# Kernel optimization log

Hardware: AMD Instinct MI355X
Metric: run time of the kernel (lower is better)

The kernel has to match this reference:

```python
import jax, jax.numpy as jnp
import numpy as np
import math

N_HEAD = 16
EPS = 1e-5
GELU_C = math.sqrt(2.0 / math.pi)

def _layernorm(v, w):
    # LN with weight only (bias=None), matching the module's quirky constructor
    mu = jnp.mean(v, axis=-1, keepdims=True)
    var = jnp.mean(jnp.square(v - mu), axis=-1, keepdims=True)
    return (v - mu) * jax.lax.rsqrt(var + EPS) * w

def _new_gelu(x):
    return 0.5 * x * (1.0 + jnp.tanh(GELU_C * (x + 0.044715 * x ** 3)))

def setup_inputs() -> dict:
    key = jax.random.key(0)
    k1, k2, k3, k4 = jax.random.split(key, 4)
    B, T, C = 2, 2048, 2048
    x = jax.random.normal(k1, (B, T, C), dtype=jnp.float32)
    w_qkv = jax.random.normal(k2, (C, 3 * C), dtype=jnp.float32) * 0.02
    w1 = jax.random.normal(k3, (C, 4 * C), dtype=jnp.float32) * 0.02
    w2 = jax.random.normal(k4, (4 * C, C), dtype=jnp.float32) * 0.02
    ln_w = jnp.ones((C,), dtype=jnp.float32)
    return {"x": x, "w_qkv": w_qkv, "w1": w1, "w2": w2, "ln_w": ln_w}

def reference(x, w_qkv, w1, w2, ln_w):
    B, T, C = x.shape
    H = N_HEAD
    D = C // H
    # --- attention branch (pre-LN, shared ln weight) ---
    h = _layernorm(x, ln_w)
    qkv = h @ w_qkv  # [B,T,3C]
    q, k, v = jnp.split(qkv, 3, axis=-1)
    q = q.reshape(B, T, H, D)
    k = k.reshape(B, T, H, D)
    v = v.reshape(B, T, H, D)
    scale = 1.0 / math.sqrt(D)
    att = jnp.einsum('bthd,bshd->bhts', q, k) * scale  # [B,H,T,T]
    causal = jnp.tril(jnp.ones((T, T), dtype=bool))
    att = jnp.where(causal, att, -jnp.inf)
    att = jax.nn.softmax(att, axis=-1)
    attn_out = jnp.einsum('bhts,bshd->bthd', att, v).reshape(B, T, C)
    x = x + attn_out  # note: no output projection in this module
    # --- MLP branch (same ln weight reused) ---
    h2 = _layernorm(x, ln_w)
    mlp = _new_gelu(h2 @ w1) @ w2
    return x + mlp
```

## Files before the change

kernel.cpp:

```cpp
#include <hip/hip_runtime.h>
#include <hip/hip_bf16.h>
#include <math.h>

typedef __bf16 BF16;
typedef __attribute__((ext_vector_type(8))) __bf16 bf16x8;
typedef __attribute__((ext_vector_type(4))) float f32x4;

__device__ __forceinline__ void gld_lds16(const void* g, void* l) {
    __builtin_amdgcn_global_load_lds(
        (__attribute__((address_space(1))) void*)(const void*)g,
        (__attribute__((address_space(3))) void*)l, 16, 0, 0);
}

template <int N> __device__ __forceinline__ void vmwait() {
    asm volatile("s_waitcnt vmcnt(%0)" :: "i"(N));
}

__global__ __launch_bounds__(256) void lnorm(const float* __restrict__ x,
                                             const float* __restrict__ w,
                                             BF16* __restrict__ out) {
    const int row = blockIdx.x, tid = threadIdx.x;
    const float* xr = x + (size_t)row * 2048;
    float4 a = *(const float4*)(xr + tid * 8);
    float4 b = *(const float4*)(xr + tid * 8 + 4);
    float s1 = a.x + a.y + a.z + a.w + b.x + b.y + b.z + b.w;
    float s2 = a.x*a.x + a.y*a.y + a.z*a.z + a.w*a.w +
               b.x*b.x + b.y*b.y + b.z*b.z + b.w*b.w;
    #pragma unroll
    for (int off = 32; off; off >>= 1) {
        s1 += __shfl_xor(s1, off);
        s2 += __shfl_xor(s2, off);
    }
    __shared__ float red[8];
    const int l = tid & 63, wv = tid >> 6;
    if (l == 0) { red[wv] = s1; red[4 + wv] = s2; }
    __syncthreads();
    s1 = red[0] + red[1] + red[2] + red[3];
    s2 = red[4] + red[5] + red[6] + red[7];
    const float mean = s1 * (1.0f / 2048.0f);
    const float var  = s2 * (1.0f / 2048.0f) - mean * mean;
    const float rstd = rsqrtf(var + 1e-5f);
    float4 wa = *(const float4*)(w + tid * 8);
    float4 wb = *(const float4*)(w + tid * 8 + 4);
    bf16x8 o;
    o[0] = (BF16)((a.x - mean) * rstd * wa.x);
    o[1] = (BF16)((a.y - mean) * rstd * wa.y);
    o[2] = (BF16)((a.z - mean) * rstd * wa.z);
    o[3] = (BF16)((a.w - mean) * rstd * wa.w);
    o[4] = (BF16)((b.x - mean) * rstd * wb.x);
    o[5] = (BF16)((b.y - mean) * rstd * wb.y);
    o[6] = (BF16)((b.z - mean) * rstd * wb.z);
    o[7] = (BF16)((b.w - mean) * rstd * wb.w);
    *(bf16x8*)(out + (size_t)row * 2048 + tid * 8) = o;
}

__global__ __launch_bounds__(256) void wtrans(const float* __restrict__ W,
                                              BF16* __restrict__ Wt,
                                              int K, int N) {
    __shared__ BF16 tile[32][33];
    const int n0 = blockIdx.x * 32, k0 = blockIdx.y * 32;
    const int tx = threadIdx.x, ty = threadIdx.y;
    #pragma unroll
    for (int i = 0; i < 4; i++)
        tile[ty + 8 * i][tx] = (BF16)W[(size_t)(k0 + ty + 8 * i) * N + n0 + tx];
    __syncthreads();
    #pragma unroll
    for (int i = 0; i < 4; i++)
        Wt[(size_t)(n0 + ty + 8 * i) * K + k0 + tx] = tile[tx][ty + 8 * i];
}

__global__ __launch_bounds__(256) void vtrans(const BF16* __restrict__ qkv,
                                              BF16* __restrict__ vT) {
    __shared__ BF16 tile[32][33];
    const int t0 = blockIdx.x * 32, d0 = blockIdx.y * 32, bh = blockIdx.z;
    const int b = bh >> 4, h = bh & 15;
    const int tx = threadIdx.x, ty = threadIdx.y;
    const BF16* src = qkv + (size_t)b * 2048 * 6144 + 4096 + h * 128;
    #pragma unroll
    for (int i = 0; i < 4; i++)
        tile[ty + 8 * i][tx] = src[(size_t)(t0 + ty + 8 * i) * 6144 + d0 + tx];
    __syncthreads();
    BF16* dst = vT + (size_t)bh * 128 * 2048;
    #pragma unroll
    for (int i = 0; i < 4; i++)
        dst[(size_t)(d0 + ty + 8 * i) * 2048 + t0 + tx] = tile[tx][ty + 8 * i];
}


#define STA(SI, TS) do { \
    _Pragma("unroll") \
    for (int j_ = 0; j_ < LA; ++j_) { \
        const int r_ = j_ * 128 + (tid >> 2); \
        const int sl_ = (tid & 3) ^ ((r_ >> 1) & 3); \
        gld_lds16(A + (size_t)(m0 + r_) * K + (TS) * 32 + sl_ * 8, \
                  Ab + (SI) * ABUF + j_ * 8192 + w * 1024); \
    } \
} while (0)

#define STB(SI, TS) do { \
    _Pragma("unroll") \
    for (int j_ = 0; j_ < 2; ++j_) { \
        const int r_ = j_ * 128 + (tid >> 2); \
        const int sl_ = (tid & 3) ^ ((r_ >> 1) & 3); \
        gld_lds16(Bt + (size_t)(n0 + r_) * K + (TS) * 32 + sl_ * 8, \
                  Bb + (SI) * 16384 + j_ * 8192 + w * 1024); \
    } \
} while (0)

#define LDA(BI, M_) \
    (*(const bf16x8*)(Ab + (BI) * ABUF + \
        (wm * (BM / 2) + (M_) * 16 + c) * 64 + ((g ^ fa) << 4)))

#define LDB(BI, N_) \
    (*(const bf16x8*)(Bb + (BI) * 16384 + \
        (wn * 64 + (N_) * 16 + c) * 64 + ((g ^ fa) << 4)))

#define GB(BI, T, DS, VW) do { \
    bf16x8 af[MR], bfr[4]; \
    _Pragma("unroll") for (int n_ = 0; n_ < 4; ++n_) bfr[n_] = LDB(BI, n_); \
    _Pragma("unroll") for (int m_ = 0; m_ < MR; ++m_) af[m_] = LDA(BI, m_); \
    if (DS) { STB(((BI) + 3) & 3, (T) + 3); STA(((BI) + 3) & 3, (T) + 3); } \
    _Pragma("unroll") \
    for (int m_ = 0; m_ < MR; ++m_) \
      _Pragma("unroll") \
      for (int n_ = 0; n_ < 4; ++n_) \
        acc[m_][n_] = __builtin_amdgcn_mfma_f32_16x16x32_bf16( \
            af[m_], bfr[n_], acc[m_][n_], 0, 0, 0); \
    vmwait<(VW)>(); \
    __builtin_amdgcn_s_barrier(); \
    __builtin_amdgcn_sched_barrier(0); \
} while (0)

template <int MODE, int BM>
__global__ __launch_bounds__(512) void gemmN(const BF16* __restrict__ A,
                                             const BF16* __restrict__ Bt,
                                             void* __restrict__ out,
                                             const float* __restrict__ resid,
                                             int M, int N, int K) {
    constexpr int MR   = BM / 32;
    constexpr int LA   = BM / 128;
    constexpr int LPT  = LA + 2;
    constexpr int ABUF = BM * 64;
    (void)M;

    extern __shared__ char smem[];
    char* const Ab = smem;
    char* const Bb = smem + 4 * ABUF;

    const int tid = threadIdx.x, l = tid & 63, w = tid >> 6;
    const int wm = w >> 2, wn = w & 3;
    const int g = l >> 4, c = l & 15;
    const int fa = (c >> 1) & 3;

    const int NBX = N >> 8;
    const int cpx = (int)gridDim.x >> 3;
    const int bid = (int)blockIdx.x;
    const int wg  = (bid & 7) * cpx + (bid >> 3);
    const int m0 = (wg / NBX) * BM, n0 = (wg % NBX) * 256;

    f32x4 acc[MR][4] = {};

    STB(0, 0); STA(0, 0);
    STB(1, 1); STA(1, 1);
    STB(2, 2); STA(2, 2);
    vmwait<2 * LPT>();
    __builtin_amdgcn_s_barrier();
    __builtin_amdgcn_sched_barrier(0);

    const int NT = K >> 5;
    for (int t = 0; t < NT - 4; t += 4) {
        GB(0, t,     1, 2 * LPT);
        GB(1, t + 1, 1, 2 * LPT);
        GB(2, t + 2, 1, 2 * LPT);
        GB(3, t + 3, 1, 2 * LPT);
    }
    GB(0, NT - 4, 1, 2 * LPT);
    GB(1, NT - 3, 0, LPT);
    GB(2, NT - 2, 0, 0);
    GB(3, NT - 1, 0, 0);

    #pragma unroll
    for (int mi = 0; mi < MR; mi++)
      #pragma unroll
      for (int ni = 0; ni < 4; ni++)
        #pragma unroll
        for (int j = 0; j < 4; j++) {
            const int row = m0 + wm * (BM / 2) + mi * 16 + g * 4 + j;
            const int col = n0 + wn * 64 + ni * 16 + c;
            const float v = acc[mi][ni][j];
            const size_t idx = (size_t)row * N + col;
            if (MODE == 0) {
                ((BF16*)out)[idx] = (BF16)v;
            } else if (MODE == 1) {
                const float t2 = v + 0.044715f * v * v * v;
                const float s = 1.0f / (1.0f + __expf(-1.5957691216057308f * t2));
                ((BF16*)out)[idx] = (BF16)(v * s);
            } else {
                ((float*)out)[idx] = resid[idx] + v;
            }
        }
}

__global__ __launch_bounds__(256) void attn(const BF16* __restrict__ qkv,
                                            const BF16* __restrict__ vT,
                                            const float* __restrict__ x,
                                            float* __restrict__ x2) {
    __shared__ BF16 Ks[2][64 * 128];
    __shared__ BF16 Vs[2][128 * 64];
    __shared__ BF16 Ps[4][16 * 72];
    const int tid = threadIdx.x, l = tid & 63, w = tid >> 6;
    const int g = l >> 4, c = l & 15;
    const int bid = (int)blockIdx.x;
    const int wg = (bid & 7) * 64 + (bid >> 3);
    const int pair = wg & 15, bh = wg >> 4;
    const int b = bh >> 4, h = bh & 15;
    const int xr = (c & 7) << 4;

    const BF16* qbase = qkv + (size_t)b * 2048 * 6144 + h * 128;
    const char* kbase = (const char*)(qbase + 2048);
    const char* vbase = (const char*)(vT + (size_t)bh * 128 * 2048);

    auto STAGE = [&](int bb, int k0) {
        #pragma unroll
        for (int s = 0; s < 4; ++s) {
            const int rK = (w * 4 + s) * 4 + (l >> 4);
            const int cK = ((l & 15) * 16) ^ ((rK & 7) << 4);
            gld_lds16(kbase + (size_t)(k0 + rK) * 12288 + cK,
                      &Ks[bb][(w * 4 + s) * 512]);
            const int rV = (w * 4 + s) * 8 + (l >> 3);
            const int cV = ((l & 7) * 16) ^ ((rV & 7) << 4);
            gld_lds16(vbase + (size_t)rV * 4096 + (size_t)k0 * 2 + cV,
                      &Vs[bb][(w * 4 + s) * 512]);
        }
    };

    const float scale = 0.08838834764831845f;

    #pragma unroll 1
    for (int seg = 0; seg < 2; ++seg) {
        const int qb = seg ? 31 - pair : pair;
        const int q0 = qb * 64;

        bf16x8 qf[4];
        {
            const BF16* qrow = qbase + (size_t)(q0 + w * 16 + c) * 6144 + g * 8;
            #pragma unroll
            for (int kc = 0; kc < 4; kc++)
                qf[kc] = *(const bf16x8*)(qrow + kc * 32);
        }
        float m[4]    = {-1e30f, -1e30f, -1e30f, -1e30f};
        float lsum[4] = {0.f, 0.f, 0.f, 0.f};
        f32x4 O[8] = {};

        STAGE(0, 0);
        #pragma unroll 1
        for (int kt = 0; kt <= qb; ++kt) {
            if (kt < qb) { STAGE((kt + 1) & 1, (kt + 1) * 64); vmwait<8>(); }
            else vmwait<0>();
            __builtin_amdgcn_s_barrier();
            __builtin_amdgcn_sched_barrier(0);
            const char* KsB = (const char*)Ks[kt & 1];
            const char* VsB = (const char*)Vs[kt & 1];

            f32x4 s4[4] = {};
            #pragma unroll
            for (int ni = 0; ni < 4; ni++)
                #pragma unroll
                for (int kc = 0; kc < 4; kc++) {
                    const bf16x8 kf = *(const bf16x8*)(KsB +
                        (ni * 16 + c) * 256 + ((kc * 64 + g * 16) ^ xr));
                    s4[ni] = __builtin_amdgcn_mfma_f32_16x16x32_bf16(
                        qf[kc], kf, s4[ni], 0, 0, 0);
                }

            const bool maskt = (kt == qb);
            float sv[4][4];
            #pragma unroll
            for (int ni = 0; ni < 4; ni++)
                #pragma unroll
                for (int j = 0; j < 4; j++) {
                    const float v = s4[ni][j] * scale;
                    sv[ni][j] = (!maskt || (ni * 16 + c <= w * 16 + g * 4 + j))
                              ? v : -1e30f;
                }

            float sf[4];
            #pragma unroll
            for (int j = 0; j < 4; j++) {
                float tm = fmaxf(fmaxf(sv[0][j], sv[1][j]),
                                 fmaxf(sv[2][j], sv[3][j]));
                tm = fmaxf(tm, __shfl_xor(tm, 1));
                tm = fmaxf(tm, __shfl_xor(tm, 2));
                tm = fmaxf(tm, __shfl_xor(tm, 4));
                tm = fmaxf(tm, __shfl_xor(tm, 8));
                const float mn = fmaxf(m[j], tm);
                sf[j] = __expf(m[j] - mn);
                m[j] = mn;
            }

            float rs[4] = {0.f, 0.f, 0.f, 0.f};
            #pragma unroll
            for (int ni = 0; ni < 4; ni++)
                #pragma unroll
                for (int j = 0; j < 4; j++) {
                    const float p = __expf(sv[ni][j] - m[j]);
                    rs[j] += p;
                    Ps[w][(g * 4 + j) * 72 + ni * 16 + c] = (BF16)p;
                }
            #pragma unroll
            for (int j = 0; j < 4; j++) {
                float t = rs[j];
                t += __shfl_xor(t, 1);
                t += __shfl_xor(t, 2);
                t += __shfl_xor(t, 4);
                t += __shfl_xor(t, 8);
                lsum[j] = lsum[j] * sf[j] + t;
            }
            #pragma unroll
            for (int dn = 0; dn < 8; dn++)
                #pragma unroll
                for (int j = 0; j < 4; j++) O[dn][j] *= sf[j];

            bf16x8 pa[2];
            #pragma unroll
            for (int ks = 0; ks < 2; ks++)
                pa[ks] = *(const bf16x8*)((const char*)Ps[w] +
                             c * 144 + ks * 64 + g * 16);
            #pragma unroll
            for (int dn = 0; dn < 8; dn++)
                #pragma unroll
                for (int ks = 0; ks < 2; ks++) {
                    const bf16x8 vf = *(const bf16x8*)(VsB +
                        (dn * 16 + c) * 128 + ((ks * 64 + g * 16) ^ xr));
                    O[dn] = __builtin_amdgcn_mfma_f32_16x16x32_bf16(
                        pa[ks], vf, O[dn], 0, 0, 0);
                }
            __builtin_amdgcn_s_barrier();
            __builtin_amdgcn_sched_barrier(0);
        }

        float inv[4];
        #pragma unroll
        for (int j = 0; j < 4; j++) inv[j] = 1.0f / lsum[j];
        #pragma unroll
        for (int dn = 0; dn < 8; dn++)
            #pragma unroll
            for (int j = 0; j < 4; j++) {
                const int t   = q0 + w * 16 + g * 4 + j;
                const int col = h * 128 + dn * 16 + c;
                const size_t idx = ((size_t)b * 2048 + t) * 2048 + col;
                x2[idx] = x[idx] + O[dn][j] * inv[j];
            }
    }
}

extern "C" void kernel_launch(void* const* d_in, const int* in_sizes, int n_in,
                              void* d_out, int out_size, void* d_ws, size_t ws_size,
                              hipStream_t stream) {
    const float* x     = (const float*)d_in[0];
    const float* w_qkv = (const float*)d_in[1];
    const float* w1    = (const float*)d_in[2];
    const float* w2    = (const float*)d_in[3];
    const float* ln_w  = (const float*)d_in[4];
    float* out = (float*)d_out;

    char* ws = (char*)d_ws;
    BF16* h_buf = (BF16*)ws;  ws += (size_t)4096 * 2048 * 2;
    BF16* qkvb  = (BF16*)ws;  ws += (size_t)4096 * 6144 * 2;
    BF16* vTb   = (BF16*)ws;  ws += (size_t)32 * 128 * 2048 * 2;
    BF16* wqkvT = (BF16*)ws;  ws += (size_t)6144 * 2048 * 2;
    BF16* w1T   = (BF16*)ws;  ws += (size_t)8192 * 2048 * 2;
    BF16* w2T   = (BF16*)ws;  ws += (size_t)2048 * 8192 * 2;
    BF16* mlp1  = (BF16*)ws;  ws += (size_t)4096 * 8192 * 2;

    hipFuncSetAttribute((const void*)&gemmN<0, 256>,
                        hipFuncAttributeMaxDynamicSharedMemorySize, 131072);
    hipFuncSetAttribute((const void*)&gemmN<1, 256>,
                        hipFuncAttributeMaxDynamicSharedMemorySize, 131072);
    hipFuncSetAttribute((const void*)&gemmN<2, 128>,
                        hipFuncAttributeMaxDynamicSharedMemorySize, 98304);

    lnorm<<<4096, 256, 0, stream>>>(x, ln_w, h_buf);
    wtrans<<<dim3(192, 64), dim3(32, 8), 0, stream>>>(w_qkv, wqkvT, 2048, 6144);
    gemmN<0, 256><<<384, 512, 131072, stream>>>(
        h_buf, wqkvT, qkvb, nullptr, 4096, 6144, 2048);
    vtrans<<<dim3(64, 4, 32), dim3(32, 8), 0, stream>>>(qkvb, vTb);
    attn<<<512, 256, 0, stream>>>(qkvb, vTb, x, out);

    lnorm<<<4096, 256, 0, stream>>>(out, ln_w, h_buf);
    wtrans<<<dim3(256, 64), dim3(32, 8), 0, stream>>>(w1, w1T, 2048, 8192);
    gemmN<1, 256><<<512, 512, 131072, stream>>>(
        h_buf, w1T, mlp1, nullptr, 4096, 8192, 2048);
    wtrans<<<dim3(64, 256), dim3(32, 8), 0, stream>>>(w2, w2T, 8192, 2048);
    gemmN<2, 128><<<256, 512, 98304, stream>>>(
        mlp1, w2T, out, out, 4096, 2048, 8192);
}
```

Before: 550.9 us.

## Replace GEMM with 256x128 tile, triple-buffered pipeline and MFMA priority

New measurement: 576.1 us. +4.6%, slower.

```diff
diff --git a/kernel.cpp b/kernel.cpp
--- a/kernel.cpp
+++ b/kernel.cpp
@@ -89,104 +89,96 @@
 
 #define STA(SI, TS) do { \
     _Pragma("unroll") \
-    for (int j_ = 0; j_ < LA; ++j_) { \
+    for (int j_ = 0; j_ < 2; ++j_) { \
         const int r_ = j_ * 128 + (tid >> 2); \
         const int sl_ = (tid & 3) ^ ((r_ >> 1) & 3); \
         gld_lds16(A + (size_t)(m0 + r_) * K + (TS) * 32 + sl_ * 8, \
-                  Ab + (SI) * ABUF + j_ * 8192 + w * 1024); \
+                  Ab + (SI) * 16384 + j_ * 8192 + w * 1024); \
     } \
 } while (0)
 
 #define STB(SI, TS) do { \
-    _Pragma("unroll") \
-    for (int j_ = 0; j_ < 2; ++j_) { \
-        const int r_ = j_ * 128 + (tid >> 2); \
+    { \
+        const int r_ = (tid >> 2); \
         const int sl_ = (tid & 3) ^ ((r_ >> 1) & 3); \
         gld_lds16(Bt + (size_t)(n0 + r_) * K + (TS) * 32 + sl_ * 8, \
-                  Bb + (SI) * 16384 + j_ * 8192 + w * 1024); \
+                  Bb + (SI) * 8192 + w * 1024); \
     } \
 } while (0)
 
 #define LDA(BI, M_) \
-    (*(const bf16x8*)(Ab + (BI) * ABUF + \
-        (wm * (BM / 2) + (M_) * 16 + c) * 64 + ((g ^ fa) << 4)))
+    (*(const bf16x8*)(Ab + (BI) * 16384 + \
+        (wm * 128 + (M_) * 16 + c) * 64 + ((g ^ fa) << 4)))
 
 #define LDB(BI, N_) \
-    (*(const bf16x8*)(Bb + (BI) * 16384 + \
-        (wn * 64 + (N_) * 16 + c) * 64 + ((g ^ fa) << 4)))
-
-#define GB(BI, T, DS, VW) do { \
-    bf16x8 af[MR], bfr[4]; \
-    _Pragma("unroll") for (int n_ = 0; n_ < 4; ++n_) bfr[n_] = LDB(BI, n_); \
-    _Pragma("unroll") for (int m_ = 0; m_ < MR; ++m_) af[m_] = LDA(BI, m_); \
-    if (DS) { STB(((BI) + 3) & 3, (T) + 3); STA(((BI) + 3) & 3, (T) + 3); } \
-    _Pragma("unroll") \
-    for (int m_ = 0; m_ < MR; ++m_) \
-      _Pragma("unroll") \
-      for (int n_ = 0; n_ < 4; ++n_) \
-        acc[m_][n_] = __builtin_amdgcn_mfma_f32_16x16x32_bf16( \
-            af[m_], bfr[n_], acc[m_][n_], 0, 0, 0); \
+    (*(const bf16x8*)(Bb + (BI) * 8192 + \
+        (wn * 32 + (N_) * 16 + c) * 64 + ((g ^ fa) << 4)))
+
+#define GB3(BI, T, ST, VW) do { \
     vmwait<(VW)>(); \
     __builtin_amdgcn_s_barrier(); \
     __builtin_amdgcn_sched_barrier(0); \
+    if (ST) { STB(((BI) + 2) % 3, (T) + 2); STA(((BI) + 2) % 3, (T) + 2); } \
+    bf16x8 bfr[2], af[8]; \
+    _Pragma("unroll") for (int n_ = 0; n_ < 2; ++n_) bfr[n_] = LDB(BI, n_); \
+    _Pragma("unroll") for (int m_ = 0; m_ < 8; ++m_) af[m_] = LDA(BI, m_); \
+    __builtin_amdgcn_s_setprio(1); \
+    _Pragma("unroll") \
+    for (int m_ = 0; m_ < 8; ++m_) \
+      _Pragma("unroll") \
+      for (int n_ = 0; n_ < 2; ++n_) \
+        acc[m_][n_] = __builtin_amdgcn_mfma_f32_16x16x32_bf16( \
+            af[m_], bfr[n_], acc[m_][n_], 0, 0, 0); \
+    __builtin_amdgcn_s_setprio(0); \
 } while (0)
 
-template <int MODE, int BM>
-__global__ __launch_bounds__(512) void gemmN(const BF16* __restrict__ A,
-                                             const BF16* __restrict__ Bt,
-                                             void* __restrict__ out,
-                                             const float* __restrict__ resid,
-                                             int M, int N, int K) {
-    constexpr int MR   = BM / 32;
-    constexpr int LA   = BM / 128;
-    constexpr int LPT  = LA + 2;
-    constexpr int ABUF = BM * 64;
+template <int MODE>
+__global__ __launch_bounds__(512, 4) void gemmP(const BF16* __restrict__ A,
+                                                const BF16* __restrict__ Bt,
+                                                void* __restrict__ out,
+                                                const float* __restrict__ resid,
+                                                int M, int N, int K) {
     (void)M;
-
     extern __shared__ char smem[];
     char* const Ab = smem;
-    char* const Bb = smem + 4 * ABUF;
+    char* const Bb = smem + 49152;
 
     const int tid = threadIdx.x, l = tid & 63, w = tid >> 6;
     const int wm = w >> 2, wn = w & 3;
     const int g = l >> 4, c = l & 15;
     const int fa = (c >> 1) & 3;
 
-    const int NBX = N >> 8;
+    const int NBX = N >> 7;
     const int cpx = (int)gridDim.x >> 3;
     const int bid = (int)blockIdx.x;
     const int wg  = (bid & 7) * cpx + (bid >> 3);
-    const int m0 = (wg / NBX) * BM, n0 = (wg % NBX) * 256;
-
-    f32x4 acc[MR][4] = {};
+    const int m0 = (wg / NBX) * 256, n0 = (wg % NBX) * 128;
+
+    f32x4 acc[8][2] = {};
 
     STB(0, 0); STA(0, 0);
     STB(1, 1); STA(1, 1);
-    STB(2, 2); STA(2, 2);
-    vmwait<2 * LPT>();
-    __builtin_amdgcn_s_barrier();
-    __builtin_amdgcn_sched_barrier(0);
 
     const int NT = K >> 5;
-    for (int t = 0; t < NT - 4; t += 4) {
-        GB(0, t,     1, 2 * LPT);
-        GB(1, t + 1, 1, 2 * LPT);
-        GB(2, t + 2, 1, 2 * LPT);
-        GB(3, t + 3, 1, 2 * LPT);
+    const int MAIN = NT - 4;
+    for (int t = 0; t < MAIN; t += 3) {
+        GB3(0, t,     1, 3);
+        GB3(1, t + 1, 1, 3);
+        GB3(2, t + 2, 1, 3);
     }
-    GB(0, NT - 4, 1, 2 * LPT);
-    GB(1, NT - 3, 0, LPT);
-    GB(2, NT - 2, 0, 0);
-    GB(3, NT - 1, 0, 0);
-
-    #pragma unroll
-    for (int mi = 0; mi < MR; mi++)
+    GB3(0, MAIN,     1, 3);
+    GB3(1, MAIN + 1, 1, 3);
+    GB3(2, MAIN + 2, 0, 3);
+    GB3(0, MAIN + 3, 0, 0);
+
+    #pragma unroll
+    for (int mi = 0; mi < 8; mi++)
       #pragma unroll
-      for (int ni = 0; ni < 4; ni++)
+      for (int ni = 0; ni < 2; ni++)
         #pragma unroll
         for (int j = 0; j < 4; j++) {
-            const int row = m0 + wm * (BM / 2) + mi * 16 + g * 4 + j;
-            const int col = n0 + wn * 64 + ni * 16 + c;
+            const int row = m0 + wm * 128 + mi * 16 + g * 4 + j;
+            const int col = n0 + wn * 32 + ni * 16 + c;
             const float v = acc[mi][ni][j];
             const size_t idx = (size_t)row * N + col;
             if (MODE == 0) {
@@ -373,25 +365,25 @@
     BF16* w2T   = (BF16*)ws;  ws += (size_t)2048 * 8192 * 2;
     BF16* mlp1  = (BF16*)ws;  ws += (size_t)4096 * 8192 * 2;
 
-    hipFuncSetAttribute((const void*)&gemmN<0, 256>,
-                        hipFuncAttributeMaxDynamicSharedMemorySize, 131072);
-    hipFuncSetAttribute((const void*)&gemmN<1, 256>,
-                        hipFuncAttributeMaxDynamicSharedMemorySize, 131072);
-    hipFuncSetAttribute((const void*)&gemmN<2, 128>,
-                        hipFuncAttributeMaxDynamicSharedMemorySize, 98304);
+    hipFuncSetAttribute((const void*)&gemmP<0>,
+                        hipFuncAttributeMaxDynamicSharedMemorySize, 73728);
+    hipFuncSetAttribute((const void*)&gemmP<1>,
+                        hipFuncAttributeMaxDynamicSharedMemorySize, 73728);
+    hipFuncSetAttribute((const void*)&gemmP<2>,
+                        hipFuncAttributeMaxDynamicSharedMemorySize, 73728);
 
     lnorm<<<4096, 256, 0, stream>>>(x, ln_w, h_buf);
     wtrans<<<dim3(192, 64), dim3(32, 8), 0, stream>>>(w_qkv, wqkvT, 2048, 6144);
-    gemmN<0, 256><<<384, 512, 131072, stream>>>(
+    gemmP<0><<<768, 512, 73728, stream>>>(
         h_buf, wqkvT, qkvb, nullptr, 4096, 6144, 2048);
     vtrans<<<dim3(64, 4, 32), dim3(32, 8), 0, stream>>>(qkvb, vTb);
     attn<<<512, 256, 0, stream>>>(qkvb, vTb, x, out);
 
     lnorm<<<4096, 256, 0, stream>>>(out, ln_w, h_buf);
     wtrans<<<dim3(256, 64), dim3(32, 8), 0, stream>>>(w1, w1T, 2048, 8192);
-    gemmN<1, 256><<<512, 512, 131072, stream>>>(
+    gemmP<1><<<1024, 512, 73728, stream>>>(
         h_buf, w1T, mlp1, nullptr, 4096, 8192, 2048);
     wtrans<<<dim3(64, 256), dim3(32, 8), 0, stream>>>(w2, w2T, 8192, 2048);
-    gemmN<2, 128><<<256, 512, 98304, stream>>>(
+    gemmP<2><<<256, 512, 73728, stream>>>(
         mlp1, w2T, out, out, 4096, 2048, 8192);
 }
```
